# Optimization experiments

Measured on AMD Instinct MI355X. Metric: run time of the kernel, lower is better.

Reference implementation:

```python
import jax, jax.numpy as jnp
import numpy as np
import math

D = 512; H = 8; NL = 6; VOCAB = 256; NC = 10; L = 1024; B = 4
DK = D // H
SCALE = math.sqrt(DK)
EMB_SCALE = math.sqrt(D)
EPS = 1e-5


def _pos_encoding(seq_len, d_model):
    pos = jnp.arange(seq_len, dtype=jnp.float32)[:, None]
    div = jnp.exp(-jnp.arange(0, d_model, 2, dtype=jnp.float32) / d_model * math.log(10000.0))
    pe = jnp.zeros((seq_len, d_model), dtype=jnp.float32)
    pe = pe.at[:, 0::2].set(jnp.sin(pos * div))
    pe = pe.at[:, 1::2].set(jnp.cos(pos * div))
    return pe


def _layer_norm(x, g, b):
    m = jnp.mean(x, axis=-1, keepdims=True)
    v = jnp.mean(jnp.square(x - m), axis=-1, keepdims=True)
    return (x - m) * jax.lax.rsqrt(v + EPS) * g + b


def setup_inputs() -> dict:
    key = jax.random.key(0)
    ks = jax.random.split(key, 18)
    s = 0.02  # keep activations in a sane range so softmax is not saturated
    return {
        "tokens": jax.random.randint(ks[0], (B, L), 0, VOCAB, dtype=jnp.int32),
        "emb_table": jax.random.normal(ks[1], (VOCAB, D), jnp.float32) * s,
        "Wq": jax.random.normal(ks[2], (NL, D, D), jnp.float32) * s,
        "bq": jax.random.normal(ks[3], (NL, D), jnp.float32) * s,
        "Wkv": jax.random.normal(ks[4], (NL, 2 * D, D), jnp.float32) * s,
        "bkv": jax.random.normal(ks[5], (NL, 2 * D), jnp.float32) * s,
        "Wo": jax.random.normal(ks[6], (NL, D, D), jnp.float32) * s,
        "bo": jax.random.normal(ks[7], (NL, D), jnp.float32) * s,
        "ln1_g": jnp.ones((NL, D), jnp.float32),
        "ln1_b": jnp.zeros((NL, D), jnp.float32),
        "W1": jax.random.normal(ks[8], (NL, 4 * D, D), jnp.float32) * s,
        "b1": jax.random.normal(ks[9], (NL, 4 * D), jnp.float32) * s,
        "W2": jax.random.normal(ks[10], (NL, D, 4 * D), jnp.float32) * s,
        "b2": jax.random.normal(ks[11], (NL, D), jnp.float32) * s,
        "ln2_g": jnp.ones((NL, D), jnp.float32),
        "ln2_b": jnp.zeros((NL, D), jnp.float32),
        "Wc": jax.random.normal(ks[12], (NC, D), jnp.float32) * s,
        "bc": jax.random.normal(ks[13], (NC,), jnp.float32) * s,
    }


def reference(tokens, emb_table, Wq, bq, Wkv, bkv, Wo, bo, ln1_g, ln1_b,
              W1, b1, W2, b2, ln2_g, ln2_b, Wc, bc):
    seq_len = tokens.shape[1]
    pe = _pos_encoding(seq_len, D)  # [L, D]
    x = emb_table[tokens] * EMB_SCALE + pe[None]  # [B, L, D]  (dropout = identity in eval)

    def block(x, p):
        wq, bq_, wkv, bkv_, wo, bo_, g1, be1, w1, bb1, w2, bb2, g2, be2 = p
        h = _layer_norm(x, g1, be1)
        q = h @ wq.T + bq_                       # [B, L, D]
        kv = h @ wkv.T + bkv_                    # [B, L, 2D]
        k, v = kv[..., :D], kv[..., D:]
        # split heads: [B, H, L, dk]
        q = q.reshape(*q.shape[:2], H, DK).transpose(0, 2, 1, 3)
        k = k.reshape(*k.shape[:2], H, DK).transpose(0, 2, 1, 3)
        v = v.reshape(*v.shape[:2], H, DK).transpose(0, 2, 1, 3)
        score = jnp.einsum('bhqd,bhkd->bhqk', q, k) / SCALE  # [B, H, L, L]
        attn = jax.nn.softmax(score, axis=-1)
        av = jnp.einsum('bhqk,bhkd->bhqd', attn, v)
        av = av.transpose(0, 2, 1, 3).reshape(*x.shape)      # merge heads
        x = x + (av @ wo.T + bo_)
        h2 = _layer_norm(x, g2, be2)
        ffn = jax.nn.relu(h2 @ w1.T + bb1) @ w2.T + bb2
        x = x + ffn
        return x, None

    params = (Wq, bq, Wkv, bkv, Wo, bo, ln1_g, ln1_b, W1, b1, W2, b2, ln2_g, ln2_b)
    x, _ = jax.lax.scan(block, x, params)
    return x @ Wc.T + bc  # [B, L, NC]
```

## Files before the change

kernel.cpp:

```cpp
#include <hip/hip_runtime.h>
#include <math.h>

#define D 512
#define HEADS 8
#define NLAYER 6
#define LSEQ 1024
#define BATCH 4
#define DKH 64
#define MTOK (BATCH*LSEQ)
#define EPS 1e-5f
#define EMB_SCALE 22.627416997969522f
#define INV_SCALE 0.125f

typedef __attribute__((ext_vector_type(8))) __bf16 bf16x8;
typedef __attribute__((ext_vector_type(4))) float f32x4;

__device__ __forceinline__ unsigned short f2bf(float x) {
    union { float f; unsigned u; } v; v.f = x;
    unsigned r = (v.u + 0x7FFFu + ((v.u >> 16) & 1u)) >> 16;
    return (unsigned short)r;
}
__device__ __forceinline__ unsigned pack2(float a, float b) {
    return (unsigned)f2bf(a) | ((unsigned)f2bf(b) << 16);
}
__device__ __forceinline__ void gl_lds16(const unsigned short* g, unsigned short* l) {
    __builtin_amdgcn_global_load_lds(
        (const __attribute__((address_space(1))) unsigned*)g,
        (__attribute__((address_space(3))) unsigned*)l, 16, 0, 0);
}
__device__ __forceinline__ void gload16(bf16x8& d, const unsigned short* p) {
    asm volatile("global_load_dwordx4 %0, %1, off" : "=v"(d) : "v"(p));
}

__global__ __launch_bounds__(256) void prep_kernel(
    const int* __restrict__ tokens, const float* __restrict__ emb,
    const float* __restrict__ Wq, const float* __restrict__ Wkv,
    const float* __restrict__ Wo, const float* __restrict__ W1,
    const float* __restrict__ W2, const float* __restrict__ bq,
    const float* __restrict__ bkv, unsigned short* __restrict__ wl,
    float* __restrict__ wbias, float* __restrict__ x)
{
    const int bid = blockIdx.x;
    if (bid < 9216) {
        const int l = bid / 1536;
        const int e = (bid - l * 1536) * 2048 + threadIdx.x * 8;
        const float* src;
        if      (e < 262144)  src = Wq  + (size_t)l * 262144  + e;
        else if (e < 786432)  src = Wkv + (size_t)l * 524288  + (e - 262144);
        else if (e < 1048576) src = Wo  + (size_t)l * 262144  + (e - 786432);
        else if (e < 2097152) src = W1  + (size_t)l * 1048576 + (e - 1048576);
        else                  src = W2  + (size_t)l * 1048576 + (e - 2097152);
        float4 a = *(const float4*)src;
        float4 b = *(const float4*)(src + 4);
        uint4 o;
        o.x = pack2(a.x, a.y); o.y = pack2(a.z, a.w);
        o.z = pack2(b.x, b.y); o.w = pack2(b.z, b.w);
        *(uint4*)(wl + (size_t)l * 3145728 + e) = o;
    } else if (bid == 9216) {
        for (int i = threadIdx.x; i < 9216; i += 256) {
            int l = i / 1536, j = i - l * 1536;
            wbias[i] = (j < 512) ? bq[l * 512 + j] : bkv[l * 1024 + (j - 512)];
        }
    } else {
        int row = (bid - 9217) * 2 + (threadIdx.x >> 7);
        int pos = row & (LSEQ - 1);
        int tok = tokens[row];
        int c = (threadIdx.x & 127) * 4;
        float4 e = *(const float4*)(emb + (size_t)tok * D + c);
        float o[4] = {e.x, e.y, e.z, e.w};
#pragma unroll
        for (int i = 0; i < 4; ++i) {
            int col = c + i;
            int ii = col & ~1;
            float dv = expf(-(float)ii * (9.210340371976184f / (float)D));
            float a = (float)pos * dv;
            float pe = (col & 1) ? cosf(a) : sinf(a);
            o[i] = o[i] * EMB_SCALE + pe;
        }
        float4 r; r.x = o[0]; r.y = o[1]; r.z = o[2]; r.w = o[3];
        *(float4*)(x + (size_t)row * D + c) = r;
    }
}

__global__ __launch_bounds__(256) void ln_kernel(
    const float* __restrict__ x, const float* __restrict__ g,
    const float* __restrict__ b, unsigned short* __restrict__ h)
{
    int lane = threadIdx.x & 63;
    int row = blockIdx.x * 4 + (threadIdx.x >> 6);
    const float* xr = x + (size_t)row * D + lane * 8;
    float4 v0 = *(const float4*)(xr);
    float4 v1 = *(const float4*)(xr + 4);
    float s = v0.x + v0.y + v0.z + v0.w + v1.x + v1.y + v1.z + v1.w;
#pragma unroll
    for (int off = 32; off; off >>= 1) s += __shfl_xor(s, off, 64);
    float m = s * (1.0f / D);
    float d0 = v0.x - m, d1 = v0.y - m, d2 = v0.z - m, d3 = v0.w - m;
    float d4 = v1.x - m, d5 = v1.y - m, d6 = v1.z - m, d7 = v1.w - m;
    float ss = d0*d0 + d1*d1 + d2*d2 + d3*d3 + d4*d4 + d5*d5 + d6*d6 + d7*d7;
#pragma unroll
    for (int off = 32; off; off >>= 1) ss += __shfl_xor(ss, off, 64);
    float inv = rsqrtf(ss * (1.0f / D) + EPS);
    const float* gp = g + lane * 8;
    const float* bp = b + lane * 8;
    float4 g0 = *(const float4*)(gp), g1 = *(const float4*)(gp + 4);
    float4 b0 = *(const float4*)(bp), b1 = *(const float4*)(bp + 4);
    uint4 o;
    o.x = pack2(d0 * inv * g0.x + b0.x, d1 * inv * g0.y + b0.y);
    o.y = pack2(d2 * inv * g0.z + b0.z, d3 * inv * g0.w + b0.w);
    o.z = pack2(d4 * inv * g1.x + b1.x, d5 * inv * g1.y + b1.y);
    o.w = pack2(d6 * inv * g1.z + b1.z, d7 * inv * g1.w + b1.w);
    *(uint4*)(h + (size_t)row * D + lane * 8) = o;
}

template<int OMODE, int BM>
__global__ __launch_bounds__(256) void gemm_bf16(
    const unsigned short* __restrict__ A, const unsigned short* __restrict__ W,
    const float* __restrict__ bias, const float* __restrict__ X,
    void* __restrict__ C, void* __restrict__ C2, void* __restrict__ C3,
    int M, int N, int K)
{
    constexpr int WM = BM / 64;
    constexpr int WN = 4 / WM;
    constexpr int NI = 8 / WN;
    __shared__ __align__(16) unsigned short As[2][BM * 64];
    __shared__ __align__(16) unsigned short Bs[2][128 * 64];
    const int tid = threadIdx.x;
    const int wave = tid >> 6, lane = tid & 63;
    const int quad = lane >> 4, l16 = lane & 15;
    const int wm = wave / WN, wn = wave % WN;
    const int bm = blockIdx.y * BM, bn = blockIdx.x * 128;

    const int rS  = tid >> 3;
    const int csw = (((tid & 7) ^ (rS & 7)) << 3);
    const unsigned short* Asrc = A + (size_t)(bm + rS) * K + csw;
    const unsigned short* Bsrc = W + (size_t)(bn + rS) * K + csw;

    f32x4 acc[4][NI];
#pragma unroll
    for (int mi = 0; mi < 4; ++mi)
#pragma unroll
        for (int ni = 0; ni < NI; ++ni) acc[mi][ni] = (f32x4){0.f, 0.f, 0.f, 0.f};

    const int nt = K >> 6;

#pragma unroll
    for (int i = 0; i < BM / 32; ++i)
        gl_lds16(Asrc + (size_t)(i * 32) * K, &As[0][i * 2048 + tid * 8]);
#pragma unroll
    for (int i = 0; i < 4; ++i)
        gl_lds16(Bsrc + (size_t)(i * 32) * K, &Bs[0][i * 2048 + tid * 8]);
    __syncthreads();

    for (int t = 0; t < nt; ++t) {
        const int cur = t & 1;
        if (t + 1 < nt) {
            const int k0 = (t + 1) << 6;
#pragma unroll
            for (int i = 0; i < BM / 32; ++i)
                gl_lds16(Asrc + (size_t)(i * 32) * K + k0, &As[cur ^ 1][i * 2048 + tid * 8]);
#pragma unroll
            for (int i = 0; i < 4; ++i)
                gl_lds16(Bsrc + (size_t)(i * 32) * K + k0, &Bs[cur ^ 1][i * 2048 + tid * 8]);
        }
#pragma unroll
        for (int kc = 0; kc < 2; ++kc) {
            const int gch = (kc << 2) | quad;
            bf16x8 af[4], bfr[NI];
#pragma unroll
            for (int mi = 0; mi < 4; ++mi) {
                const int ra = wm * 64 + mi * 16 + l16;
                af[mi] = *(const bf16x8*)&As[cur][ra * 64 + ((gch ^ (ra & 7)) << 3)];
            }
#pragma unroll
            for (int ni = 0; ni < NI; ++ni) {
                const int rb = wn * (128 / WN) + ni * 16 + l16;
                bfr[ni] = *(const bf16x8*)&Bs[cur][rb * 64 + ((gch ^ (rb & 7)) << 3)];
            }
#pragma unroll
            for (int mi = 0; mi < 4; ++mi)
#pragma unroll
                for (int ni = 0; ni < NI; ++ni)
                    acc[mi][ni] = __builtin_amdgcn_mfma_f32_16x16x32_bf16(
                        af[mi], bfr[ni], acc[mi][ni], 0, 0, 0);
        }
        __syncthreads();
    }

    const int er = bm + wm * 64;
    const int ec = bn + wn * (128 / WN);

    if (OMODE == 0) {
        float* Cf = (float*)C;
#pragma unroll
        for (int ni = 0; ni < NI; ++ni) {
            int c = ec + ni * 16 + l16;
            float bv = bias[c];
#pragma unroll
            for (int mi = 0; mi < 4; ++mi)
#pragma unroll
                for (int r = 0; r < 4; ++r) {
                    int m = er + mi * 16 + quad * 4 + r;
                    Cf[(size_t)m * N + c] = acc[mi][ni][r] + bv + X[(size_t)m * N + c];
                }
        }
    } else if (OMODE == 1) {
        unsigned short* Cb = (unsigned short*)C;
#pragma unroll
        for (int ni = 0; ni < NI; ++ni) {
            int c = ec + ni * 16 + l16;
            float bv = bias[c];
#pragma unroll
            for (int mi = 0; mi < 4; ++mi)
#pragma unroll
                for (int r = 0; r < 4; ++r) {
                    int m = er + mi * 16 + quad * 4 + r;
                    Cb[(size_t)m * N + c] = f2bf(fmaxf(acc[mi][ni][r] + bv, 0.f));
                }
        }
    } else {
        if (bn < 512) {
            unsigned short* Qp = (unsigned short*)C;
#pragma unroll
            for (int ni = 0; ni < NI; ++ni) {
                int c = ec + ni * 16 + l16;
                float bv = bias[c];
                int hh = c >> 6, dd = c & 63;
                size_t cbase = (size_t)(dd >> 5) * 512 + (size_t)((dd >> 3) & 3) * 128 + (dd & 7);
#pragma unroll
                for (int mi = 0; mi < 4; ++mi)
#pragma unroll
                    for (int r = 0; r < 4; ++r) {
                        int m = er + mi * 16 + quad * 4 + r;
                        int b = m >> 10, t = m & 1023;
                        Qp[(size_t)(b * 8 + hh) * 65536 + (size_t)(t >> 4) * 1024
                           + cbase + (size_t)(t & 15) * 8] =
                            f2bf((acc[mi][ni][r] + bv) * INV_SCALE);
                    }
            }
        } else if (bn < 1024) {
            unsigned short* Kp = (unsigned short*)C2;
#pragma unroll
            for (int ni = 0; ni < NI; ++ni) {
                int c = ec + ni * 16 + l16;
                float bv = bias[c];
                int c2 = c - 512;
                int hh = c2 >> 6, dd = c2 & 63;
                size_t cbase = (size_t)(dd >> 5) * 512 + (size_t)((dd >> 3) & 3) * 128 + (dd & 7);
#pragma unroll
                for (int mi = 0; mi < 4; ++mi)
#pragma unroll
                    for (int r = 0; r < 4; ++r) {
                        int m = er + mi * 16 + quad * 4 + r;
                        int b = m >> 10, t = m & 1023;
                        Kp[(size_t)(b * 8 + hh) * 65536 + (size_t)(t >> 4) * 1024
                           + cbase + (size_t)(t & 15) * 8] =
                            f2bf(acc[mi][ni][r] + bv);
                    }
            }
        } else {
            unsigned short* Vp = (unsigned short*)C3;
#pragma unroll
            for (int ni = 0; ni < NI; ++ni) {
                int c = ec + ni * 16 + l16;
                float bv = bias[c];
                int c2 = c - 1024;
                int hh = c2 >> 6, dd = c2 & 63;
                size_t dbase = (size_t)(dd >> 4) * 16384 + (size_t)(dd & 15) * 8;
#pragma unroll
                for (int mi = 0; mi < 4; ++mi) {
                    int t0 = er + mi * 16 + quad * 4;
                    int b = t0 >> 10, tt = t0 & 1023;
                    ushort4 o;
                    o.x = f2bf(acc[mi][ni][0] + bv);
                    o.y = f2bf(acc[mi][ni][1] + bv);
                    o.z = f2bf(acc[mi][ni][2] + bv);
                    o.w = f2bf(acc[mi][ni][3] + bv);
                    *(ushort4*)(Vp + (size_t)(b * 8 + hh) * 65536 + dbase
                                + (size_t)(tt >> 5) * 512
                                + (size_t)((tt >> 3) & 3) * 128 + (tt & 7)) = o;
                }
            }
        }
    }
}

__global__ __launch_bounds__(256, 1) void attn_mfma(
    const unsigned short* __restrict__ Qb, const unsigned short* __restrict__ Kb,
    const unsigned short* __restrict__ Vt, unsigned short* __restrict__ av)
{
    __shared__ float Ol[4][32][68];
    __shared__ float Ls[4][32];
    const int tid = threadIdx.x;
    const int wave = tid >> 6, lane = tid & 63;
    const int quad = lane >> 4, l16 = lane & 15;
    const int bh = blockIdx.x & 31;
    const int b = bh >> 3, h = bh & 7;
    const int q0 = (blockIdx.x >> 5) * 32;

    const unsigned short* qp = Qb + (size_t)bh * 65536 + (size_t)(q0 >> 4) * 1024 + lane * 8;
    const unsigned short* kbase = Kb + (size_t)bh * 65536 + lane * 8;
    const unsigned short* vbase = Vt + (size_t)bh * 65536 + lane * 8;

    const int sA  = ((((2 * quad) & 3) << 4) + l16) << 2;
    const int sB2 = ((((2 * quad + 1) & 3) << 4) + l16) << 2;

    f32x4 o[2][4];
#pragma unroll
    for (int qs = 0; qs < 2; ++qs)
#pragma unroll
        for (int nf = 0; nf < 4; ++nf) o[qs][nf] = (f32x4){0.f, 0.f, 0.f, 0.f};
    float lp[2] = {0.f, 0.f};

    const int j0 = wave * 256;

    bf16x8 qf[2][2];
    gload16(qf[0][0], qp);
    gload16(qf[0][1], qp + 512);
    gload16(qf[1][0], qp + 1024);
    gload16(qf[1][1], qp + 1536);

    bf16x8 kc[2][8], vf[2][8];
#pragma unroll
    for (int nf = 0; nf < 4; ++nf) {
        gload16(kc[0][2 * nf],     kbase + (size_t)j0 * 64 + nf * 1024);
        gload16(kc[0][2 * nf + 1], kbase + (size_t)j0 * 64 + nf * 1024 + 512);
        gload16(vf[0][2 * nf],     vbase + (size_t)j0 * 16 + nf * 16384);
        gload16(vf[0][2 * nf + 1], vbase + (size_t)j0 * 16 + nf * 16384 + 512);
    }

#pragma unroll
    for (int it = 0; it < 4; ++it) {
        const int cur = it & 1, nxt = cur ^ 1;
        if (it < 3) {
            const int jn = j0 + (it + 1) * 64;
#pragma unroll
            for (int nf = 0; nf < 4; ++nf) {
                gload16(kc[nxt][2 * nf],     kbase + (size_t)jn * 64 + nf * 1024);
                gload16(kc[nxt][2 * nf + 1], kbase + (size_t)jn * 64 + nf * 1024 + 512);
                gload16(vf[nxt][2 * nf],     vbase + (size_t)jn * 16 + nf * 16384);
                gload16(vf[nxt][2 * nf + 1], vbase + (size_t)jn * 16 + nf * 16384 + 512);
            }
        }
        if (it < 3) asm volatile("s_waitcnt vmcnt(16)" ::: "memory");
        else        asm volatile("s_waitcnt vmcnt(0)"  ::: "memory");
        __builtin_amdgcn_sched_barrier(0);
        unsigned pk01[2][4], pk23[2][4];
#pragma unroll
        for (int nf = 0; nf < 4; ++nf)
#pragma unroll
            for (int qs = 0; qs < 2; ++qs) {
                f32x4 z = {0.f, 0.f, 0.f, 0.f};
                z = __builtin_amdgcn_mfma_f32_16x16x32_bf16(kc[cur][2 * nf], qf[qs][0], z, 0, 0, 0);
                z = __builtin_amdgcn_mfma_f32_16x16x32_bf16(kc[cur][2 * nf + 1], qf[qs][1], z, 0, 0, 0);
                float p0 = __expf(z[0]);
                float p1 = __expf(z[1]);
                float p2 = __expf(z[2]);
                float p3 = __expf(z[3]);
                lp[qs] += (p0 + p1) + (p2 + p3);
                pk01[qs][nf] = pack2(p0, p1);
                pk23[qs][nf] = pack2(p2, p3);
            }
#pragma unroll
        for (int qs = 0; qs < 2; ++qs) {
            union PU { unsigned d[4]; bf16x8 v; } f0, f1;
            unsigned a0, a1;
            a0 = (unsigned)__builtin_amdgcn_ds_bpermute(sA,  (int)pk01[qs][0]);
            a1 = (unsigned)__builtin_amdgcn_ds_bpermute(sA,  (int)pk01[qs][1]);
            f0.d[0] = (quad < 2) ? a0 : a1;
            a0 = (unsigned)__builtin_amdgcn_ds_bpermute(sA,  (int)pk23[qs][0]);
            a1 = (unsigned)__builtin_amdgcn_ds_bpermute(sA,  (int)pk23[qs][1]);
            f0.d[1] = (quad < 2) ? a0 : a1;
            a0 = (unsigned)__builtin_amdgcn_ds_bpermute(sB2, (int)pk01[qs][0]);
            a1 = (unsigned)__builtin_amdgcn_ds_bpermute(sB2, (int)pk01[qs][1]);
            f0.d[2] = (quad < 2) ? a0 : a1;
            a0 = (unsigned)__builtin_amdgcn_ds_bpermute(sB2, (int)pk23[qs][0]);
            a1 = (unsigned)__builtin_amdgcn_ds_bpermute(sB2, (int)pk23[qs][1]);
            f0.d[3] = (quad < 2) ? a0 : a1;
            a0 = (unsigned)__builtin_amdgcn_ds_bpermute(sA,  (int)pk01[qs][2]);
            a1 = (unsigned)__builtin_amdgcn_ds_bpermute(sA,  (int)pk01[qs][3]);
            f1.d[0] = (quad < 2) ? a0 : a1;
            a0 = (unsigned)__builtin_amdgcn_ds_bpermute(sA,  (int)pk23[qs][2]);
            a1 = (unsigned)__builtin_amdgcn_ds_bpermute(sA,  (int)pk23[qs][3]);
            f1.d[1] = (quad < 2) ? a0 : a1;
            a0 = (unsigned)__builtin_amdgcn_ds_bpermute(sB2, (int)pk01[qs][2]);
            a1 = (unsigned)__builtin_amdgcn_ds_bpermute(sB2, (int)pk01[qs][3]);
            f1.d[2] = (quad < 2) ? a0 : a1;
            a0 = (unsigned)__builtin_amdgcn_ds_bpermute(sB2, (int)pk23[qs][2]);
            a1 = (unsigned)__builtin_amdgcn_ds_bpermute(sB2, (int)pk23[qs][3]);
            f1.d[3] = (quad < 2) ? a0 : a1;
#pragma unroll
            for (int nf = 0; nf < 4; ++nf) {
                o[qs][nf] = __builtin_amdgcn_mfma_f32_16x16x32_bf16(f0.v, vf[cur][2 * nf], o[qs][nf], 0, 0, 0);
                o[qs][nf] = __builtin_amdgcn_mfma_f32_16x16x32_bf16(f1.v, vf[cur][2 * nf + 1], o[qs][nf], 0, 0, 0);
            }
        }
    }
#pragma unroll
    for (int qs = 0; qs < 2; ++qs)
#pragma unroll
        for (int nf = 0; nf < 4; ++nf)
#pragma unroll
            for (int r = 0; r < 4; ++r)
                Ol[wave][qs * 16 + quad * 4 + r][nf * 16 + l16] = o[qs][nf][r];
#pragma unroll
    for (int qs = 0; qs < 2; ++qs) {
        float ts = lp[qs];
        ts += __shfl_xor(ts, 16, 64);
        ts += __shfl_xor(ts, 32, 64);
        if (quad == 0) Ls[wave][qs * 16 + l16] = ts;
    }
    __syncthreads();
#pragma unroll
    for (int half = 0; half < 2; ++half)
#pragma unroll
        for (int r = 0; r < 4; ++r) {
            int qq = half * 16 + quad * 4 + r;
            float denom = Ls[0][qq] + Ls[1][qq] + Ls[2][qq] + Ls[3][qq];
            float v = Ol[0][qq][wave * 16 + l16] + Ol[1][qq][wave * 16 + l16]
                    + Ol[2][qq][wave * 16 + l16] + Ol[3][qq][wave * 16 + l16];
            int q = q0 + qq;
            av[((size_t)(b * 1024 + q)) * D + h * 64 + wave * 16 + l16] =
                f2bf(v / denom);
        }
}

__global__ __launch_bounds__(256) void cls_kernel(
    const float* __restrict__ x, const float* __restrict__ Wc,
    const float* __restrict__ bc, float* __restrict__ out)
{
    int lane = threadIdx.x & 63;
    int row = blockIdx.x * 4 + (threadIdx.x >> 6);
    const float* xr = x + (size_t)row * D + lane * 8;
    float4 v0 = *(const float4*)xr;
    float4 v1 = *(const float4*)(xr + 4);
    float acc[10];
#pragma unroll
    for (int c = 0; c < 10; ++c) {
        const float* wr = Wc + c * D + lane * 8;
        float4 w0 = *(const float4*)wr;
        float4 w1 = *(const float4*)(wr + 4);
        acc[c] = v0.x*w0.x + v0.y*w0.y + v0.z*w0.z + v0.w*w0.w
               + v1.x*w1.x + v1.y*w1.y + v1.z*w1.z + v1.w*w1.w;
    }
#pragma unroll
    for (int c = 0; c < 10; ++c)
#pragma unroll
        for (int off = 32; off; off >>= 1) acc[c] += __shfl_xor(acc[c], off, 64);
    if (lane == 0) {
#pragma unroll
        for (int c = 0; c < 10; ++c) out[(size_t)row * 10 + c] = acc[c] + bc[c];
    }
}

extern "C" void kernel_launch(void* const* d_in, const int* in_sizes, int n_in,
                              void* d_out, int out_size, void* d_ws, size_t ws_size,
                              hipStream_t stream)
{
    const int*   tokens = (const int*)  d_in[0];
    const float* emb    = (const float*)d_in[1];
    const float* Wq     = (const float*)d_in[2];
    const float* bq     = (const float*)d_in[3];
    const float* Wkv    = (const float*)d_in[4];
    const float* bkv    = (const float*)d_in[5];
    const float* Wo     = (const float*)d_in[6];
    const float* bo     = (const float*)d_in[7];
    const float* ln1g   = (const float*)d_in[8];
    const float* ln1b   = (const float*)d_in[9];
    const float* W1     = (const float*)d_in[10];
    const float* b1     = (const float*)d_in[11];
    const float* W2     = (const float*)d_in[12];
    const float* b2     = (const float*)d_in[13];
    const float* ln2g   = (const float*)d_in[14];
    const float* ln2b   = (const float*)d_in[15];
    const float* Wc     = (const float*)d_in[16];
    const float* bc     = (const float*)d_in[17];
    float* out = (float*)d_out;

    float* x  = (float*)d_ws;
    unsigned short* hb  = (unsigned short*)(x + (size_t)MTOK * D);
    unsigned short* Qb  = hb  + (size_t)MTOK * D;
    unsigned short* Kb  = Qb  + (size_t)32 * 1024 * 64;
    unsigned short* Vt  = Kb  + (size_t)32 * 1024 * 64;
    unsigned short* avb = Vt  + (size_t)32 * 1024 * 64;
    unsigned short* f1b = Qb;
    unsigned short* wl  = avb + (size_t)32 * 1024 * 64;
    float* wbias = (float*)(wl + (size_t)6 * 3145728);

    const size_t oWo = 786432, oW1 = 1048576, oW2 = 2097152, LW = 3145728;

    prep_kernel<<<11265, 256, 0, stream>>>(
        tokens, emb, Wq, Wkv, Wo, W1, W2, bq, bkv, wl, wbias, x);

    for (int l = 0; l < NLAYER; ++l) {
        const unsigned short* wll = wl + (size_t)l * LW;
        ln_kernel<<<MTOK / 4, 256, 0, stream>>>(x, ln1g + l * D, ln1b + l * D, hb);
        gemm_bf16<2,128><<<dim3(12, 32), 256, 0, stream>>>(
            hb, wll, wbias + l * 1536, nullptr, Qb, Kb, Vt, MTOK, 1536, 512);
        attn_mfma<<<1024, 256, 0, stream>>>(Qb, Kb, Vt, avb);
        gemm_bf16<0,64><<<dim3(4, 64), 256, 0, stream>>>(
            avb, wll + oWo, bo + l * D, x, x, nullptr, nullptr, MTOK, D, D);
        ln_kernel<<<MTOK / 4, 256, 0, stream>>>(x, ln2g + l * D, ln2b + l * D, hb);
        gemm_bf16<1,128><<<dim3(16, 32), 256, 0, stream>>>(
            hb, wll + oW1, b1 + l * 4 * D, nullptr, f1b, nullptr, nullptr, MTOK, 4 * D, D);
        gemm_bf16<0,64><<<dim3(4, 64), 256, 0, stream>>>(
            f1b, wll + oW2, b2 + l * D, x, x, nullptr, nullptr, MTOK, D, 4 * D);
    }

    cls_kernel<<<MTOK / 4, 256, 0, stream>>>(x, Wc, bc, out);
}
```

Baseline: 789.5 us.

## Fuse LayerNorm into GEMM A-loads using row stats accumulated in epilogues

Removes the standalone LayerNorm kernels. Residual-writing GEMM epilogues (and the embedding prep) now accumulate per-row sum and sum-of-squares via shuffles and atomics. The consuming GEMMs read fp32 x, normalize with those stats and write bf16 into LDS in place of the async global-to-LDS A copy. This saves launches and the bf16 h round trip through memory. In exchange it adds atomics in the epilogue, register-staged A loads with more fp32 traffic that is repeated across N tiles, and a one-pass variance formula that is less numerically stable.

```diff
diff --git a/kernel.cpp b/kernel.cpp
--- a/kernel.cpp
+++ b/kernel.cpp
@@ -38,7 +38,8 @@
     const float* __restrict__ Wo, const float* __restrict__ W1,
     const float* __restrict__ W2, const float* __restrict__ bq,
     const float* __restrict__ bkv, unsigned short* __restrict__ wl,
-    float* __restrict__ wbias, float* __restrict__ x)
+    float* __restrict__ wbias, float* __restrict__ stats,
+    float* __restrict__ x)
 {
     const int bid = blockIdx.x;
     if (bid < 9216) {
@@ -61,68 +62,57 @@
             int l = i / 1536, j = i - l * 1536;
             wbias[i] = (j < 512) ? bq[l * 512 + j] : bkv[l * 1024 + (j - 512)];
         }
+    } else if (bid < 9313) {
+        int i = (bid - 9217) * 1024 + threadIdx.x * 4;
+        *(float4*)&stats[8192 + i] = (float4){0.f, 0.f, 0.f, 0.f};
     } else {
-        int row = (bid - 9217) * 2 + (threadIdx.x >> 7);
+        int row = (bid - 9313) * 4 + (threadIdx.x >> 6);
+        int lane = threadIdx.x & 63;
         int pos = row & (LSEQ - 1);
         int tok = tokens[row];
-        int c = (threadIdx.x & 127) * 4;
-        float4 e = *(const float4*)(emb + (size_t)tok * D + c);
-        float o[4] = {e.x, e.y, e.z, e.w};
-#pragma unroll
-        for (int i = 0; i < 4; ++i) {
-            int col = c + i;
-            int ii = col & ~1;
+        int c = lane * 8;
+        const float* ep = emb + (size_t)tok * D + c;
+        float4 e0 = *(const float4*)ep;
+        float4 e1 = *(const float4*)(ep + 4);
+        float v[8] = {e0.x, e0.y, e0.z, e0.w, e1.x, e1.y, e1.z, e1.w};
+        float s = 0.f, ss = 0.f;
+#pragma unroll
+        for (int i = 0; i < 8; ++i) {
+            int col = c + i, ii = col & ~1;
             float dv = expf(-(float)ii * (9.210340371976184f / (float)D));
             float a = (float)pos * dv;
             float pe = (col & 1) ? cosf(a) : sinf(a);
-            o[i] = o[i] * EMB_SCALE + pe;
-        }
-        float4 r; r.x = o[0]; r.y = o[1]; r.z = o[2]; r.w = o[3];
-        *(float4*)(x + (size_t)row * D + c) = r;
-    }
-}
-
-__global__ __launch_bounds__(256) void ln_kernel(
-    const float* __restrict__ x, const float* __restrict__ g,
-    const float* __restrict__ b, unsigned short* __restrict__ h)
-{
-    int lane = threadIdx.x & 63;
-    int row = blockIdx.x * 4 + (threadIdx.x >> 6);
-    const float* xr = x + (size_t)row * D + lane * 8;
-    float4 v0 = *(const float4*)(xr);
-    float4 v1 = *(const float4*)(xr + 4);
-    float s = v0.x + v0.y + v0.z + v0.w + v1.x + v1.y + v1.z + v1.w;
-#pragma unroll
-    for (int off = 32; off; off >>= 1) s += __shfl_xor(s, off, 64);
-    float m = s * (1.0f / D);
-    float d0 = v0.x - m, d1 = v0.y - m, d2 = v0.z - m, d3 = v0.w - m;
-    float d4 = v1.x - m, d5 = v1.y - m, d6 = v1.z - m, d7 = v1.w - m;
-    float ss = d0*d0 + d1*d1 + d2*d2 + d3*d3 + d4*d4 + d5*d5 + d6*d6 + d7*d7;
-#pragma unroll
-    for (int off = 32; off; off >>= 1) ss += __shfl_xor(ss, off, 64);
-    float inv = rsqrtf(ss * (1.0f / D) + EPS);
-    const float* gp = g + lane * 8;
-    const float* bp = b + lane * 8;
-    float4 g0 = *(const float4*)(gp), g1 = *(const float4*)(gp + 4);
-    float4 b0 = *(const float4*)(bp), b1 = *(const float4*)(bp + 4);
-    uint4 o;
-    o.x = pack2(d0 * inv * g0.x + b0.x, d1 * inv * g0.y + b0.y);
-    o.y = pack2(d2 * inv * g0.z + b0.z, d3 * inv * g0.w + b0.w);
-    o.z = pack2(d4 * inv * g1.x + b1.x, d5 * inv * g1.y + b1.y);
-    o.w = pack2(d6 * inv * g1.z + b1.z, d7 * inv * g1.w + b1.w);
-    *(uint4*)(h + (size_t)row * D + lane * 8) = o;
-}
-
-template<int OMODE, int BM>
+            v[i] = v[i] * EMB_SCALE + pe;
+            s += v[i]; ss += v[i] * v[i];
+        }
+        float4 r0; r0.x = v[0]; r0.y = v[1]; r0.z = v[2]; r0.w = v[3];
+        float4 r1; r1.x = v[4]; r1.y = v[5]; r1.z = v[6]; r1.w = v[7];
+        *(float4*)(x + (size_t)row * D + c) = r0;
+        *(float4*)(x + (size_t)row * D + c + 4) = r1;
+#pragma unroll
+        for (int off = 1; off < 64; off <<= 1) {
+            s  += __shfl_xor(s,  off, 64);
+            ss += __shfl_xor(ss, off, 64);
+        }
+        if (lane == 0) { stats[row * 2] = s; stats[row * 2 + 1] = ss; }
+    }
+}
+
+template<int OMODE, int BM, int LNA>
 __global__ __launch_bounds__(256) void gemm_bf16(
-    const unsigned short* __restrict__ A, const unsigned short* __restrict__ W,
+    const unsigned short* __restrict__ A,
+    const float* __restrict__ Ax, const float* __restrict__ lstats,
+    const float* __restrict__ lg, const float* __restrict__ lb,
+    const unsigned short* __restrict__ W,
     const float* __restrict__ bias, const float* __restrict__ X,
     void* __restrict__ C, void* __restrict__ C2, void* __restrict__ C3,
+    float* __restrict__ statsOut,
     int M, int N, int K)
 {
     constexpr int WM = BM / 64;
     constexpr int WN = 4 / WM;
     constexpr int NI = 8 / WN;
+    constexpr int LPTA = BM / 32;
     __shared__ __align__(16) unsigned short As[2][BM * 64];
     __shared__ __align__(16) unsigned short Bs[2][128 * 64];
     const int tid = threadIdx.x;
@@ -133,7 +123,6 @@
 
     const int rS  = tid >> 3;
     const int csw = (((tid & 7) ^ (rS & 7)) << 3);
-    const unsigned short* Asrc = A + (size_t)(bm + rS) * K + csw;
     const unsigned short* Bsrc = W + (size_t)(bn + rS) * K + csw;
 
     f32x4 acc[4][NI];
@@ -144,25 +133,7 @@
 
     const int nt = K >> 6;
 
-#pragma unroll
-    for (int i = 0; i < BM / 32; ++i)
-        gl_lds16(Asrc + (size_t)(i * 32) * K, &As[0][i * 2048 + tid * 8]);
-#pragma unroll
-    for (int i = 0; i < 4; ++i)
-        gl_lds16(Bsrc + (size_t)(i * 32) * K, &Bs[0][i * 2048 + tid * 8]);
-    __syncthreads();
-
-    for (int t = 0; t < nt; ++t) {
-        const int cur = t & 1;
-        if (t + 1 < nt) {
-            const int k0 = (t + 1) << 6;
-#pragma unroll
-            for (int i = 0; i < BM / 32; ++i)
-                gl_lds16(Asrc + (size_t)(i * 32) * K + k0, &As[cur ^ 1][i * 2048 + tid * 8]);
-#pragma unroll
-            for (int i = 0; i < 4; ++i)
-                gl_lds16(Bsrc + (size_t)(i * 32) * K + k0, &Bs[cur ^ 1][i * 2048 + tid * 8]);
-        }
+    auto COMPUTE = [&](int cur) {
 #pragma unroll
         for (int kc = 0; kc < 2; ++kc) {
             const int gch = (kc << 2) | quad;
@@ -184,7 +155,84 @@
                     acc[mi][ni] = __builtin_amdgcn_mfma_f32_16x16x32_bf16(
                         af[mi], bfr[ni], acc[mi][ni], 0, 0, 0);
         }
+    };
+    auto BSTAGE = [&](int t, int buf) {
+        const int k0 = t << 6;
+#pragma unroll
+        for (int i = 0; i < 4; ++i)
+            gl_lds16(Bsrc + (size_t)(i * 32) * K + k0, &Bs[buf][i * 2048 + tid * 8]);
+    };
+
+    if constexpr (LNA) {
+        float meanv[LPTA], invv[LPTA];
+#pragma unroll
+        for (int i = 0; i < LPTA; ++i) {
+            float sm = lstats[(size_t)(bm + rS + i * 32) * 2];
+            float sq = lstats[(size_t)(bm + rS + i * 32) * 2 + 1];
+            float mm = sm * (1.0f / D);
+            meanv[i] = mm;
+            invv[i]  = rsqrtf(sq * (1.0f / D) - mm * mm + EPS);
+        }
+        float4 xv[LPTA][2], gv[2], bvv[2];
+        auto XLOAD = [&](int t) {
+            const int col = csw + (t << 6);
+            gv[0]  = *(const float4*)(lg + col);
+            gv[1]  = *(const float4*)(lg + col + 4);
+            bvv[0] = *(const float4*)(lb + col);
+            bvv[1] = *(const float4*)(lb + col + 4);
+#pragma unroll
+            for (int i = 0; i < LPTA; ++i) {
+                const float* xr = Ax + (size_t)(bm + rS + i * 32) * K + col;
+                xv[i][0] = *(const float4*)xr;
+                xv[i][1] = *(const float4*)(xr + 4);
+            }
+        };
+        auto XWRITE = [&](int buf) {
+#pragma unroll
+            for (int i = 0; i < LPTA; ++i) {
+                float mm = meanv[i], iv = invv[i];
+                uint4 o;
+                o.x = pack2((xv[i][0].x - mm) * iv * gv[0].x + bvv[0].x,
+                            (xv[i][0].y - mm) * iv * gv[0].y + bvv[0].y);
+                o.y = pack2((xv[i][0].z - mm) * iv * gv[0].z + bvv[0].z,
+                            (xv[i][0].w - mm) * iv * gv[0].w + bvv[0].w);
+                o.z = pack2((xv[i][1].x - mm) * iv * gv[1].x + bvv[1].x,
+                            (xv[i][1].y - mm) * iv * gv[1].y + bvv[1].y);
+                o.w = pack2((xv[i][1].z - mm) * iv * gv[1].z + bvv[1].z,
+                            (xv[i][1].w - mm) * iv * gv[1].w + bvv[1].w);
+                *(uint4*)&As[buf][i * 2048 + tid * 8] = o;
+            }
+        };
+        XLOAD(0);
+        BSTAGE(0, 0);
+        XWRITE(0);
         __syncthreads();
+        for (int t = 0; t < nt; ++t) {
+            const int cur = t & 1;
+            if (t + 1 < nt) { XLOAD(t + 1); BSTAGE(t + 1, cur ^ 1); }
+            COMPUTE(cur);
+            if (t + 1 < nt) XWRITE(cur ^ 1);
+            __syncthreads();
+        }
+    } else {
+        const unsigned short* Asrc = A + (size_t)(bm + rS) * K + csw;
+#pragma unroll
+        for (int i = 0; i < LPTA; ++i)
+            gl_lds16(Asrc + (size_t)(i * 32) * K, &As[0][i * 2048 + tid * 8]);
+        BSTAGE(0, 0);
+        __syncthreads();
+        for (int t = 0; t < nt; ++t) {
+            const int cur = t & 1;
+            if (t + 1 < nt) {
+                const int k0 = (t + 1) << 6;
+#pragma unroll
+                for (int i = 0; i < LPTA; ++i)
+                    gl_lds16(Asrc + (size_t)(i * 32) * K + k0, &As[cur ^ 1][i * 2048 + tid * 8]);
+                BSTAGE(t + 1, cur ^ 1);
+            }
+            COMPUTE(cur);
+            __syncthreads();
+        }
     }
 
     const int er = bm + wm * 64;
@@ -193,17 +241,28 @@
     if (OMODE == 0) {
         float* Cf = (float*)C;
 #pragma unroll
-        for (int ni = 0; ni < NI; ++ni) {
-            int c = ec + ni * 16 + l16;
-            float bv = bias[c];
-#pragma unroll
-            for (int mi = 0; mi < 4; ++mi)
-#pragma unroll
-                for (int r = 0; r < 4; ++r) {
-                    int m = er + mi * 16 + quad * 4 + r;
-                    Cf[(size_t)m * N + c] = acc[mi][ni][r] + bv + X[(size_t)m * N + c];
+        for (int mi = 0; mi < 4; ++mi)
+#pragma unroll
+            for (int r = 0; r < 4; ++r) {
+                int m = er + mi * 16 + quad * 4 + r;
+                float s = 0.f, sq = 0.f;
+#pragma unroll
+                for (int ni = 0; ni < NI; ++ni) {
+                    int c = ec + ni * 16 + l16;
+                    float val = acc[mi][ni][r] + bias[c] + X[(size_t)m * N + c];
+                    Cf[(size_t)m * N + c] = val;
+                    s += val; sq += val * val;
                 }
-        }
+#pragma unroll
+                for (int off = 1; off < 16; off <<= 1) {
+                    s  += __shfl_xor(s,  off, 64);
+                    sq += __shfl_xor(sq, off, 64);
+                }
+                if (l16 == 0) {
+                    atomicAdd(&statsOut[(size_t)m * 2],     s);
+                    atomicAdd(&statsOut[(size_t)m * 2 + 1], sq);
+                }
+            }
     } else if (OMODE == 1) {
         unsigned short* Cb = (unsigned short*)C;
 #pragma unroll
@@ -486,25 +545,32 @@
     unsigned short* f1b = Qb;
     unsigned short* wl  = avb + (size_t)32 * 1024 * 64;
     float* wbias = (float*)(wl + (size_t)6 * 3145728);
+    float* stats = wbias + 9216;
 
     const size_t oWo = 786432, oW1 = 1048576, oW2 = 2097152, LW = 3145728;
 
-    prep_kernel<<<11265, 256, 0, stream>>>(
-        tokens, emb, Wq, Wkv, Wo, W1, W2, bq, bkv, wl, wbias, x);
+    prep_kernel<<<10337, 256, 0, stream>>>(
+        tokens, emb, Wq, Wkv, Wo, W1, W2, bq, bkv, wl, wbias, stats, x);
 
     for (int l = 0; l < NLAYER; ++l) {
         const unsigned short* wll = wl + (size_t)l * LW;
-        ln_kernel<<<MTOK / 4, 256, 0, stream>>>(x, ln1g + l * D, ln1b + l * D, hb);
-        gemm_bf16<2,128><<<dim3(12, 32), 256, 0, stream>>>(
-            hb, wll, wbias + l * 1536, nullptr, Qb, Kb, Vt, MTOK, 1536, 512);
+        float* s_ln1  = stats + (size_t)l * 8192;
+        float* s_ln1n = stats + (size_t)(l + 1) * 8192;
+        float* s_ln2  = stats + (size_t)(7 + l) * 8192;
+        gemm_bf16<2, 128, 1><<<dim3(12, 32), 256, 0, stream>>>(
+            nullptr, x, s_ln1, ln1g + l * D, ln1b + l * D,
+            wll, wbias + l * 1536, nullptr, Qb, Kb, Vt, nullptr, MTOK, 1536, 512);
         attn_mfma<<<1024, 256, 0, stream>>>(Qb, Kb, Vt, avb);
-        gemm_bf16<0,64><<<dim3(4, 64), 256, 0, stream>>>(
-            avb, wll + oWo, bo + l * D, x, x, nullptr, nullptr, MTOK, D, D);
-        ln_kernel<<<MTOK / 4, 256, 0, stream>>>(x, ln2g + l * D, ln2b + l * D, hb);
-        gemm_bf16<1,128><<<dim3(16, 32), 256, 0, stream>>>(
-            hb, wll + oW1, b1 + l * 4 * D, nullptr, f1b, nullptr, nullptr, MTOK, 4 * D, D);
-        gemm_bf16<0,64><<<dim3(4, 64), 256, 0, stream>>>(
-            f1b, wll + oW2, b2 + l * D, x, x, nullptr, nullptr, MTOK, D, 4 * D);
+        gemm_bf16<0, 64, 0><<<dim3(4, 64), 256, 0, stream>>>(
+            avb, nullptr, nullptr, nullptr, nullptr,
+            wll + oWo, bo + l * D, x, x, nullptr, nullptr, s_ln2, MTOK, D, D);
+        gemm_bf16<1, 128, 1><<<dim3(16, 32), 256, 0, stream>>>(
+            nullptr, x, s_ln2, ln2g + l * D, ln2b + l * D,
+            wll + oW1, b1 + l * 4 * D, nullptr, f1b, nullptr, nullptr, nullptr,
+            MTOK, 4 * D, D);
+        gemm_bf16<0, 64, 0><<<dim3(4, 64), 256, 0, stream>>>(
+            f1b, nullptr, nullptr, nullptr, nullptr,
+            wll + oW2, b2 + l * D, x, x, nullptr, nullptr, s_ln1n, MTOK, D, 4 * D);
     }
 
     cls_kernel<<<MTOK / 4, 256, 0, stream>>>(x, Wc, bc, out);
```

After: 1.021 ms. 29.3% more time.
